# Optimization experiments

Hardware: AMD Instinct MI355X
Metric: run time of the kernel (lower is better)

The kernel has to match this reference:

```python
import jax, jax.numpy as jnp
import numpy as np

L, E, K = 2, 8, 2  # num_layers, num_experts, top_k
B, S, I, H = 4, 512, 768, 768


def gru_seq(x_seq, h0, Wih, Whh, bih, bhh):
    """PyTorch-semantics GRU over [B,S,H]. Returns (outputs [B,S,H], h_last [B,H])."""
    def step(h, x_t):
        gi = x_t @ Wih.T + bih          # [B,3H]
        gh = h @ Whh.T + bhh            # [B,3H]
        i_r, i_z, i_n = jnp.split(gi, 3, axis=-1)
        h_r, h_z, h_n = jnp.split(gh, 3, axis=-1)
        r = jax.nn.sigmoid(i_r + h_r)
        z = jax.nn.sigmoid(i_z + h_z)
        n = jnp.tanh(i_n + r * h_n)
        h_new = (1.0 - z) * n + z * h
        return h_new, h_new
    h_last, ys = jax.lax.scan(step, h0, jnp.swapaxes(x_seq, 0, 1))  # scan over S
    return jnp.swapaxes(ys, 0, 1), h_last


def setup_inputs() -> dict:
    key = jax.random.key(0)
    ks = jax.random.split(key, 16)
    sc_in = 1.0 / np.sqrt(I)
    sc_h = 1.0 / np.sqrt(H)
    sc_ff = 1.0 / np.sqrt(4 * I)
    return {
        "x": jax.random.normal(ks[0], (B, S, I), jnp.float32),
        "proj_W": jax.random.normal(ks[1], (L, H, I), jnp.float32) * sc_in,
        "proj_b": jnp.zeros((L, H), jnp.float32),
        "gru_Wih": jax.random.normal(ks[2], (3 * H, H), jnp.float32) * sc_h,
        "gru_Whh": jax.random.normal(ks[3], (3 * H, H), jnp.float32) * sc_h,
        "gru_bih": jnp.zeros((3 * H,), jnp.float32),
        "gru_bhh": jnp.zeros((3 * H,), jnp.float32),
        "router_W": jax.random.normal(ks[4], (L, E, H), jnp.float32) * sc_h,
        "router_b": jnp.zeros((L, E), jnp.float32),
        "exp_W1": jax.random.normal(ks[5], (L, E, 4 * I, I), jnp.float32) * sc_in,
        "exp_b1": jnp.zeros((L, E, 4 * I), jnp.float32),
        "exp_W2": jax.random.normal(ks[6], (L, E, I, 4 * I), jnp.float32) * sc_ff,
        "exp_b2": jnp.zeros((L, E, I), jnp.float32),
    }


def reference(x, proj_W, proj_b, gru_Wih, gru_Whh, gru_bih, gru_bhh,
              router_W, router_b, exp_W1, exp_b1, exp_W2, exp_b2):
    h_state = jnp.zeros((B, H), x.dtype)  # GRU state carried across layers
    for l in range(L):
        # layer projection -> recurrent router state
        h_in = x @ proj_W[l].T + proj_b[l]                       # [B,S,H]
        h_seq, h_state = gru_seq(h_in, h_state, gru_Wih, gru_Whh, gru_bih, gru_bhh)
        # top-k routing over experts
        logits = h_seq @ router_W[l].T + router_b[l]             # [B,S,E]
        vals, idx = jax.lax.top_k(logits, K)                     # [B,S,K]
        gates_k = jax.nn.softmax(vals, axis=-1)                  # renormalized over top-k
        gate = jnp.sum(gates_k[..., None] * jax.nn.one_hot(idx, E, dtype=x.dtype), axis=-2)  # [B,S,E]
        # dense-masked expert compute (small fixed E)
        out = jnp.zeros_like(x)
        for e in range(E):
            h1 = jax.nn.relu(x @ exp_W1[l, e].T + exp_b1[l, e])  # [B,S,4I]
            ye = h1 @ exp_W2[l, e].T + exp_b2[l, e]              # [B,S,I]
            out = out + gate[..., e:e + 1] * ye
        x = out
    return x
```

## Files before the change

### kernel.cpp

```cpp
#include <hip/hip_runtime.h>
#include <cmath>

#define AGENT __HIP_MEMORY_SCOPE_AGENT


typedef __attribute__((ext_vector_type(8))) short short8;
typedef __attribute__((ext_vector_type(4))) float f32x4;

__global__ void reset_kernel(int* __restrict__ flags, int* __restrict__ counts,
                             float* __restrict__ hbuf0) {
  int i = blockIdx.x * 256 + threadIdx.x;
  if (i < 6208) flags[i] = 0;
  if (i < 16) counts[i] = 0;
  if (i < 3072) hbuf0[i] = 0.f;
}

__global__ __launch_bounds__(256)
void split_kernel(const float* __restrict__ in, short* __restrict__ hi,
                  short* __restrict__ lo, int n4) {
  int i = blockIdx.x * 256 + threadIdx.x;
  if (i >= n4) return;
  float4 v = ((const float4*)in)[i];
  unsigned ua = __float_as_uint(v.x), ub = __float_as_uint(v.y);
  unsigned uc = __float_as_uint(v.z), ud = __float_as_uint(v.w);
  unsigned ha = ua & 0xFFFF0000u, hb = ub & 0xFFFF0000u;
  unsigned hc = uc & 0xFFFF0000u, hd = ud & 0xFFFF0000u;
  unsigned hp0 = (ua >> 16) | hb;
  unsigned hp1 = (uc >> 16) | hd;
  float la = v.x - __uint_as_float(ha), lb = v.y - __uint_as_float(hb);
  float lc = v.z - __uint_as_float(hc), ld = v.w - __uint_as_float(hd);
  unsigned lp0 = (__float_as_uint(la) >> 16) | (__float_as_uint(lb) & 0xFFFF0000u);
  unsigned lp1 = (__float_as_uint(lc) >> 16) | (__float_as_uint(ld) & 0xFFFF0000u);
  ((uint2*)hi)[i] = make_uint2(hp0, hp1);
  ((uint2*)lo)[i] = make_uint2(lp0, lp1);
}

template<bool GI2>
__global__ __launch_bounds__(256)
void gemm_nt(const float* __restrict__ A, const float* __restrict__ Bw,
             const float* __restrict__ bias, float* __restrict__ C,
             int Kd, int lda, int ldc)
{
  __shared__ float As[16][132];
  __shared__ float Bs[16][132];

  int mbase = blockIdx.y * 128;
  int nbase = blockIdx.x * 128;
  int tid = threadIdx.x;
  int tx = tid & 15, ty = tid >> 4;

  const float* ap[2];
  const float* bp[2];
  int ldst[2];
#pragma unroll
  for (int i = 0; i < 2; ++i) {
    int v = tid + 256 * i;
    int row = v >> 2, kq = v & 3;
    ap[i] = A + (size_t)(mbase + row) * lda + kq * 4;
    bp[i] = Bw + (size_t)(nbase + row) * Kd + kq * 4;
    ldst[i] = kq * 4 * 132 + row;
  }

  float acc[8][8];
#pragma unroll
  for (int i = 0; i < 8; ++i)
#pragma unroll
    for (int j = 0; j < 8; ++j) acc[i][j] = 0.f;

  for (int kb = 0; kb < Kd; kb += 16) {
    float4 av[2], bv[2];
#pragma unroll
    for (int i = 0; i < 2; ++i) {
      av[i] = *(const float4*)(ap[i] + kb);
      bv[i] = *(const float4*)(bp[i] + kb);
    }
    if (kb) __syncthreads();
#pragma unroll
    for (int i = 0; i < 2; ++i) {
      float* ad = &As[0][0] + ldst[i];
      ad[0] = av[i].x; ad[132] = av[i].y; ad[264] = av[i].z; ad[396] = av[i].w;
      float* bd = &Bs[0][0] + ldst[i];
      bd[0] = bv[i].x; bd[132] = bv[i].y; bd[264] = bv[i].z; bd[396] = bv[i].w;
    }
    __syncthreads();
#pragma unroll
    for (int kk = 0; kk < 16; ++kk) {
      float a[8], b[8];
      *(float4*)&a[0] = *(const float4*)&As[kk][ty * 4];
      *(float4*)&a[4] = *(const float4*)&As[kk][ty * 4 + 64];
      *(float4*)&b[0] = *(const float4*)&Bs[kk][tx * 4];
      *(float4*)&b[4] = *(const float4*)&Bs[kk][tx * 4 + 64];
#pragma unroll
      for (int i = 0; i < 8; ++i)
#pragma unroll
        for (int j = 0; j < 8; ++j)
          acc[i][j] = fmaf(a[i], b[j], acc[i][j]);
    }
  }

#pragma unroll
  for (int i = 0; i < 8; ++i) {
    int lrow = ty * 4 + (i & 3) + ((i >> 2) << 6);
    int grow = mbase + lrow;
#pragma unroll
    for (int q = 0; q < 2; ++q) {
      int col = nbase + tx * 4 + (q << 6);
      float4 bb = *(const float4*)&bias[col];
      float4 st = make_float4(acc[i][q * 4 + 0] + bb.x, acc[i][q * 4 + 1] + bb.y,
                              acc[i][q * 4 + 2] + bb.z, acc[i][q * 4 + 3] + bb.w);
      if constexpr (GI2) {
        int t = grow & 511, bb2 = grow >> 9;
        int gate = col / 768, jj = col - gate * 768;
        int wg2 = jj >> 3, o = jj & 7;
        float* dst = C + ((((size_t)t * 96 + wg2) * 4 + bb2) * 3 + gate) * 8 + o;
        *(float4*)dst = st;
      } else {
        *(float4*)&C[(size_t)grow * ldc + col] = st;
      }
    }
  }
}

template<bool SHIFT, bool RELU, bool GATE, bool OUTSPLIT>
__global__ __launch_bounds__(256)
void gemm_mfma(const short* __restrict__ Ah_g, const short* __restrict__ Al_g,
               const float* __restrict__ Bw, const float* __restrict__ bias,
               float* __restrict__ C, short* __restrict__ Ch,
               short* __restrict__ Cl, int Kd, int lda, int ldc,
               const int* __restrict__ list, const int* __restrict__ count,
               const float* __restrict__ gates, long wstride, int bstride)
{
  __shared__ __align__(16) short Ah[128][40];
  __shared__ __align__(16) short Al[128][40];
  __shared__ __align__(16) short Bh[128][40];
  __shared__ __align__(16) short Bl[128][40];
  __shared__ int rowlist[128];

  int e = blockIdx.z;
  int cnt = count[e];
  int mbase = blockIdx.y * 128;
  if (mbase >= cnt) return;
  int nbase = blockIdx.x * 128;
  const float* Bp = Bw + (size_t)e * (size_t)wstride;
  const float* biasp = bias + (size_t)e * (size_t)bstride;

  int tid = threadIdx.x;
  if (tid < 128) {
    int r = mbase + tid;
    rowlist[tid] = list[e * 4096 + (r < cnt ? r : cnt - 1)];
  }
  __syncthreads();

  int arow = tid >> 1, ahalf = tid & 1;
  int aidx0 = rowlist[arow];
  int sr = SHIFT ? (aidx0 >> 1) : aidx0;
  const short* aph = Ah_g + (size_t)sr * lda + ahalf * 16;
  const short* apl = Al_g + (size_t)sr * lda + ahalf * 16;
  const float* bp = Bp + (size_t)(nbase + arow) * Kd + ahalf * 16;

  int wave = tid >> 6, lane = tid & 63;
  int wr = (wave >> 1) * 64, wc = (wave & 1) * 64;
  int fr = lane & 15, fo = (lane >> 4) * 8;

  f32x4 acc[4][4];
#pragma unroll
  for (int i = 0; i < 4; ++i)
#pragma unroll
    for (int j = 0; j < 4; ++j) acc[i][j] = f32x4{0.f, 0.f, 0.f, 0.f};

  for (int kb = 0; kb < Kd; kb += 32) {
    uint4 a_h0 = *(const uint4*)(aph + kb);
    uint4 a_h1 = *(const uint4*)(aph + kb + 8);
    uint4 a_l0 = *(const uint4*)(apl + kb);
    uint4 a_l1 = *(const uint4*)(apl + kb + 8);
    float4 b0 = *(const float4*)(bp + kb);
    float4 b1 = *(const float4*)(bp + kb + 4);
    float4 b2 = *(const float4*)(bp + kb + 8);
    float4 b3 = *(const float4*)(bp + kb + 12);
    if (kb) __syncthreads();
    *(uint4*)&Ah[arow][ahalf * 16] = a_h0;
    *(uint4*)&Ah[arow][ahalf * 16 + 8] = a_h1;
    *(uint4*)&Al[arow][ahalf * 16] = a_l0;
    *(uint4*)&Al[arow][ahalf * 16 + 8] = a_l1;
    unsigned hp[8], lp[8];
    const float4 bbv[4] = {b0, b1, b2, b3};
#pragma unroll
    for (int q = 0; q < 4; ++q) {
      unsigned ua = __float_as_uint(bbv[q].x), ub = __float_as_uint(bbv[q].y);
      unsigned uc = __float_as_uint(bbv[q].z), ud = __float_as_uint(bbv[q].w);
      unsigned ha = ua & 0xFFFF0000u, hb = ub & 0xFFFF0000u;
      unsigned hc = uc & 0xFFFF0000u, hd = ud & 0xFFFF0000u;
      hp[q * 2] = (ua >> 16) | hb;
      hp[q * 2 + 1] = (uc >> 16) | hd;
      float la = bbv[q].x - __uint_as_float(ha);
      float lb = bbv[q].y - __uint_as_float(hb);
      float lc = bbv[q].z - __uint_as_float(hc);
      float ld = bbv[q].w - __uint_as_float(hd);
      lp[q * 2] = (__float_as_uint(la) >> 16) | (__float_as_uint(lb) & 0xFFFF0000u);
      lp[q * 2 + 1] = (__float_as_uint(lc) >> 16) | (__float_as_uint(ld) & 0xFFFF0000u);
    }
    *(uint4*)&Bh[arow][ahalf * 16] = make_uint4(hp[0], hp[1], hp[2], hp[3]);
    *(uint4*)&Bh[arow][ahalf * 16 + 8] = make_uint4(hp[4], hp[5], hp[6], hp[7]);
    *(uint4*)&Bl[arow][ahalf * 16] = make_uint4(lp[0], lp[1], lp[2], lp[3]);
    *(uint4*)&Bl[arow][ahalf * 16 + 8] = make_uint4(lp[4], lp[5], lp[6], lp[7]);
    __syncthreads();

    short8 fah[4], fal[4], fbh[4], fbl[4];
#pragma unroll
    for (int mt = 0; mt < 4; ++mt) {
      fah[mt] = *(const short8*)&Ah[wr + mt * 16 + fr][fo];
      fal[mt] = *(const short8*)&Al[wr + mt * 16 + fr][fo];
    }
#pragma unroll
    for (int nt = 0; nt < 4; ++nt) {
      fbh[nt] = *(const short8*)&Bh[wc + nt * 16 + fr][fo];
      fbl[nt] = *(const short8*)&Bl[wc + nt * 16 + fr][fo];
    }
#pragma unroll
    for (int mt = 0; mt < 4; ++mt)
#pragma unroll
      for (int nt = 0; nt < 4; ++nt) {
        acc[mt][nt] = __builtin_amdgcn_mfma_f32_16x16x32_bf16(fah[mt], fbh[nt], acc[mt][nt], 0, 0, 0);
        acc[mt][nt] = __builtin_amdgcn_mfma_f32_16x16x32_bf16(fah[mt], fbl[nt], acc[mt][nt], 0, 0, 0);
        acc[mt][nt] = __builtin_amdgcn_mfma_f32_16x16x32_bf16(fal[mt], fbh[nt], acc[mt][nt], 0, 0, 0);
      }
  }

  int crow = (lane >> 4) * 4;
#pragma unroll
  for (int mt = 0; mt < 4; ++mt) {
#pragma unroll
    for (int q = 0; q < 4; ++q) {
      int lrow = wr + mt * 16 + crow + q;
      int grow = mbase + lrow;
      if (grow < cnt) {
        int aidx = rowlist[lrow];
#pragma unroll
        for (int nt = 0; nt < 4; ++nt) {
          int col = nbase + wc + nt * 16 + fr;
          float v = acc[mt][nt][q] + biasp[col];
          if (RELU) v = fmaxf(v, 0.f);
          if (GATE) v *= gates[aidx];
          if (OUTSPLIT) {
            unsigned u = __float_as_uint(v);
            unsigned h = u & 0xFFFF0000u;
            Ch[(size_t)aidx * ldc + col] = (short)(u >> 16);
            float l2 = v - __uint_as_float(h);
            Cl[(size_t)aidx * ldc + col] = (short)(__float_as_uint(l2) >> 16);
          } else {
            C[(size_t)aidx * ldc + col] = v;
          }
        }
      }
    }
  }
}

__global__ __launch_bounds__(512)
void gru_kernel(const float* __restrict__ gi2, float* __restrict__ h_seq,
                float* __restrict__ hbuf, const float* __restrict__ Whh,
                const float* __restrict__ bhh,
                int* __restrict__ tags, int stepBase)
{
  const int H = 768, S = 512;
  __shared__ float hs[3072];
  int wg = blockIdx.x;
  int tid = threadIdx.x;
  int wave = tid >> 6;
  int lane = tid & 63;
  int j = wg * 8 + wave;

  float W[3][12];
#pragma unroll
  for (int g = 0; g < 3; ++g) {
    const float* wp = Whh + (size_t)(g * H + j) * H + lane * 4;
    *(float4*)&W[g][0] = *(const float4*)(wp);
    *(float4*)&W[g][4] = *(const float4*)(wp + 256);
    *(float4*)&W[g][8] = *(const float4*)(wp + 512);
  }
  float bh_r = bhh[j], bh_z = bhh[H + j], bh_n = bhh[2 * H + j];

  float h_own = 0.f;
  if (lane < 4)
    h_own = __hip_atomic_load(&hbuf[(stepBase & 1) * 3072 + lane * H + j],
                              __ATOMIC_RELAXED, AGENT);

  for (int tl = 0; tl < S; ++tl) {
    int g = stepBase + tl;
    const float* hb = hbuf + (g & 1) * 3072;
    float* hw = hbuf + ((g + 1) & 1) * 3072;

    float gv = 0.f;
    if (lane < 12)
      gv = gi2[(((size_t)tl * 96 + wg) * 12 + ((lane & 3) * 3 + (lane >> 2))) * 8 + wave];

    if (wave == 0) {
      for (;;) {
        int v1 = __hip_atomic_load(&tags[lane * 32], __ATOMIC_RELAXED, AGENT);
        int v2 = (lane < 32)
            ? __hip_atomic_load(&tags[(64 + lane) * 32], __ATOMIC_RELAXED, AGENT)
            : 0x7fffffff;
        if (__all(v1 >= g && v2 >= g)) break;
        __builtin_amdgcn_s_sleep(4);
      }
    }
    __syncthreads();

    float4 a, b4v;
    asm volatile("global_load_dwordx4 %0, %1, off sc0 sc1"
                 : "=v"(a) : "v"(hb + tid * 4) : "memory");
    if (tid < 256)
      asm volatile("global_load_dwordx4 %0, %1, off sc0 sc1"
                   : "=v"(b4v) : "v"(hb + 2048 + tid * 4) : "memory");
    asm volatile("s_waitcnt vmcnt(0)" ::: "memory");
    __builtin_amdgcn_sched_barrier(0);
    *(float4*)&hs[tid * 4] = a;
    if (tid < 256) *(float4*)&hs[2048 + tid * 4] = b4v;
    __syncthreads();

    if (tl >= 1) {
      if (wg < 64) {
        int rel = tid - wg * 8;
        if (rel >= 0 && rel < 8) {
          int i0 = tid * 4, bb = i0 / 768, d = i0 - bb * 768;
          *(float4*)&h_seq[((size_t)bb * S + (tl - 1)) * H + d] = a;
        }
      } else {
        int rel = tid - (wg - 64) * 8;
        if (rel >= 0 && rel < 8) {
          int i1 = 2048 + tid * 4, bb1 = i1 / 768, d1 = i1 - bb1 * 768;
          *(float4*)&h_seq[((size_t)bb1 * S + (tl - 1)) * H + d1] = b4v;
        }
      }
    }

    float hseg[4][12];
#pragma unroll
    for (int b4 = 0; b4 < 4; ++b4) {
      *(float4*)&hseg[b4][0] = *(const float4*)&hs[b4 * 768 + lane * 4];
      *(float4*)&hseg[b4][4] = *(const float4*)&hs[b4 * 768 + 256 + lane * 4];
      *(float4*)&hseg[b4][8] = *(const float4*)&hs[b4 * 768 + 512 + lane * 4];
    }

    float acc[3][4];
#pragma unroll
    for (int gg = 0; gg < 3; ++gg)
#pragma unroll
      for (int b4 = 0; b4 < 4; ++b4) {
        float s = 0.f;
#pragma unroll
        for (int i = 0; i < 12; ++i) s = fmaf(W[gg][i], hseg[b4][i], s);
        acc[gg][b4] = s;
      }
#pragma unroll
    for (int gg = 0; gg < 3; ++gg)
#pragma unroll
      for (int b4 = 0; b4 < 4; ++b4) {
        float v = acc[gg][b4];
#pragma unroll
        for (int m = 32; m >= 1; m >>= 1) v += __shfl_xor(v, m);
        acc[gg][b4] = v;
      }

    float gi_r = __shfl(gv, (lane & 3));
    float gi_z = __shfl(gv, 4 + (lane & 3));
    float gi_n = __shfl(gv, 8 + (lane & 3));

    if (lane < 4) {
      float ar = acc[0][0], az = acc[1][0], an = acc[2][0];
      if (lane == 1) { ar = acc[0][1]; az = acc[1][1]; an = acc[2][1]; }
      if (lane == 2) { ar = acc[0][2]; az = acc[1][2]; an = acc[2][2]; }
      if (lane == 3) { ar = acc[0][3]; az = acc[1][3]; an = acc[2][3]; }
      float r = 1.f / (1.f + expf(-(gi_r + ar + bh_r)));
      float z = 1.f / (1.f + expf(-(gi_z + az + bh_z)));
      float n = tanhf(gi_n + r * (an + bh_n));
      float hn = (1.f - z) * n + z * h_own;
      h_own = hn;
      __hip_atomic_store(&hw[lane * H + j], hn, __ATOMIC_RELAXED, AGENT);
    }

    asm volatile("s_waitcnt vmcnt(0)" ::: "memory");
    __syncthreads();
    if (tid == 0)
      __hip_atomic_store(&tags[wg * 32], g + 1, __ATOMIC_RELAXED, AGENT);
  }

  if (lane < 4)
    h_seq[((size_t)lane * S + (S - 1)) * H + j] = h_own;
}

__global__ __launch_bounds__(64)
void router_kernel(const float* __restrict__ h_seq, const float* __restrict__ rW,
                   const float* __restrict__ rb, int* __restrict__ counts,
                   int* __restrict__ lists, float* __restrict__ gates)
{
  int t = blockIdx.x;
  int lane = threadIdx.x;
  const float* hp = h_seq + (size_t)t * 768 + lane * 12;
  float h[12];
  *(float4*)&h[0] = *(const float4*)(hp);
  *(float4*)&h[4] = *(const float4*)(hp + 4);
  *(float4*)&h[8] = *(const float4*)(hp + 8);

  float lg[8];
#pragma unroll
  for (int e = 0; e < 8; ++e) {
    const float* wp = rW + e * 768 + lane * 12;
    float s = 0.f;
#pragma unroll
    for (int i = 0; i < 12; ++i) s = fmaf(h[i], wp[i], s);
#pragma unroll
    for (int m = 32; m >= 1; m >>= 1) s += __shfl_xor(s, m);
    lg[e] = s + rb[e];
  }
  if (lane == 0) {
    float v1 = lg[0]; int e1 = 0;
#pragma unroll
    for (int e = 1; e < 8; ++e) {
      if (lg[e] > v1) { v1 = lg[e]; e1 = e; }
    }
    float v2 = -INFINITY; int es = 0;
#pragma unroll
    for (int e = 0; e < 8; ++e) {
      if (e != e1 && lg[e] > v2) { v2 = lg[e]; es = e; }
    }
    float ed = expf(v2 - v1);
    float g1 = 1.f / (1.f + ed);
    float g2 = ed / (1.f + ed);
    int a0 = t * 2, a1 = t * 2 + 1;
    gates[a0] = g1;
    gates[a1] = g2;
    int p = atomicAdd(&counts[e1], 1);
    lists[e1 * 4096 + p] = a0;
    p = atomicAdd(&counts[es], 1);
    lists[es * 4096 + p] = a1;
  }
}

__global__ __launch_bounds__(256)
void combine_kernel(const float* __restrict__ ybuf, float* __restrict__ out)
{
  int i = blockIdx.x * 256 + threadIdx.x;
  int fi = i * 4;
  int t = fi / 768;
  int d = fi % 768;
  float4 y0 = *(const float4*)&ybuf[(size_t)(2 * t) * 768 + d];
  float4 y1 = *(const float4*)&ybuf[(size_t)(2 * t + 1) * 768 + d];
  float4 r = make_float4(y0.x + y1.x, y0.y + y1.y, y0.z + y1.z, y0.w + y1.w);
  *(float4*)&out[fi] = r;
}

extern "C" void kernel_launch(void* const* d_in, const int* in_sizes, int n_in,
                              void* d_out, int out_size, void* d_ws, size_t ws_size,
                              hipStream_t stream) {
  (void)in_sizes; (void)n_in; (void)out_size; (void)ws_size;
  const float* x      = (const float*)d_in[0];
  const float* proj_W = (const float*)d_in[1];
  const float* proj_b = (const float*)d_in[2];
  const float* Wih    = (const float*)d_in[3];
  const float* Whh    = (const float*)d_in[4];
  const float* bih    = (const float*)d_in[5];
  const float* bhh    = (const float*)d_in[6];
  const float* rW     = (const float*)d_in[7];
  const float* rb     = (const float*)d_in[8];
  const float* eW1    = (const float*)d_in[9];
  const float* eb1    = (const float*)d_in[10];
  const float* eW2    = (const float*)d_in[11];
  const float* eb2    = (const float*)d_in[12];
  float* out = (float*)d_out;

  float* f = (float*)d_ws;
  float* h_in  = f;
  float* gi2   = h_in + 1572864;
  float* h_seq = gi2 + 4718592;
  float* x_buf = h_seq + 1572864;
  float* ybuf  = x_buf + 1572864;
  float* hbuf  = ybuf + 3145728;
  float* gates = hbuf + 6144;
  short* xh    = (short*)(gates + 4096);
  short* xl    = xh + 1572864;
  short* H1h   = xl + 1572864;
  short* H1l   = H1h + 12582912;
  int* ints    = (int*)(H1l + 12582912);
  int* counts  = ints;
  int* lists   = ints + 16;
  int* tags    = ints + 16 + 32768;

  reset_kernel<<<25, 256, 0, stream>>>(tags, counts, hbuf);

  for (int l = 0; l < 2; ++l) {
    const float* xin = l ? x_buf : x;

    dim3 g1(6, 16);
    gemm_nt<false><<<g1, 256, 0, stream>>>(
        xin, proj_W + (size_t)l * 768 * 768, proj_b + l * 768, h_in,
        768, 768, 768);

    dim3 g2(18, 16);
    gemm_nt<true><<<g2, 256, 0, stream>>>(
        h_in, Wih, bih, gi2, 768, 768, 0);

    gru_kernel<<<96, 512, 0, stream>>>(gi2, h_seq, hbuf, Whh, bhh,
                                       tags, l * 512);

    router_kernel<<<2048, 64, 0, stream>>>(h_seq, rW + (size_t)l * 8 * 768,
                                           rb + l * 8, counts + l * 8, lists, gates);

    split_kernel<<<1536, 256, 0, stream>>>(xin, xh, xl, 393216);

    dim3 ga(24, 32, 8);
    gemm_mfma<true, true, false, true><<<ga, 256, 0, stream>>>(
        xh, xl, eW1 + (size_t)l * 8 * 3072 * 768, eb1 + (size_t)l * 8 * 3072,
        nullptr, H1h, H1l, 768, 768, 3072,
        lists, counts + l * 8, nullptr, (long)3072 * 768, 3072);

    dim3 gb(6, 32, 8);
    gemm_mfma<false, false, true, false><<<gb, 256, 0, stream>>>(
        H1h, H1l, eW2 + (size_t)l * 8 * 768 * 3072, eb2 + (size_t)l * 8 * 768,
        ybuf, nullptr, nullptr, 3072, 3072, 768,
        lists, counts + l * 8, gates, (long)768 * 3072, 768);

    combine_kernel<<<1536, 256, 0, stream>>>(ybuf, l ? out : x_buf);
  }
}
```

Baseline: 6.070 ms.

## Partition GRU workgroups by batch to shrink cross-block synchronization groups

The GRU recurrence kernel now assigns each batch row to its own group of 24 workgroups, each wave computing 4 hidden columns for one batch instead of one column for all 4 batches. Each workgroup then polls only 24 peer flags instead of 96 and loads only its batch's 768-element hidden state per step, which cuts the per-step barrier and load cost on the latency-bound serial loop. The gi projection layout is rearranged to match, and the sleep interval in the spin loop is shortened. In exchange each wave holds four times as many Whh weights in registers, which raises register pressure, and each weight row is now read by four batch groups.

```diff
diff --git a/kernel.cpp b/kernel.cpp
--- a/kernel.cpp
+++ b/kernel.cpp
@@ -35,7 +35,7 @@
   ((uint2*)lo)[i] = make_uint2(lp0, lp1);
 }
 
-template<bool GI2>
+template<bool GI3>
 __global__ __launch_bounds__(256)
 void gemm_nt(const float* __restrict__ A, const float* __restrict__ Bw,
              const float* __restrict__ bias, float* __restrict__ C,
@@ -108,11 +108,11 @@
       float4 bb = *(const float4*)&bias[col];
       float4 st = make_float4(acc[i][q * 4 + 0] + bb.x, acc[i][q * 4 + 1] + bb.y,
                               acc[i][q * 4 + 2] + bb.z, acc[i][q * 4 + 3] + bb.w);
-      if constexpr (GI2) {
+      if constexpr (GI3) {
         int t = grow & 511, bb2 = grow >> 9;
         int gate = col / 768, jj = col - gate * 768;
-        int wg2 = jj >> 3, o = jj & 7;
-        float* dst = C + ((((size_t)t * 96 + wg2) * 4 + bb2) * 3 + gate) * 8 + o;
+        int wv = jj >> 2;
+        float* dst = C + ((((size_t)t * 4 + bb2) * 192 + wv) * 12 + gate * 4);
         *(float4*)dst = st;
       } else {
         *(float4*)&C[(size_t)grow * ldc + col] = st;
@@ -256,110 +256,95 @@
   }
 }
 
-__global__ __launch_bounds__(512)
-void gru_kernel(const float* __restrict__ gi2, float* __restrict__ h_seq,
+__global__ __launch_bounds__(512, 2)
+void gru_kernel(const float* __restrict__ gi3, float* __restrict__ h_seq,
                 float* __restrict__ hbuf, const float* __restrict__ Whh,
                 const float* __restrict__ bhh,
                 int* __restrict__ tags, int stepBase)
 {
   const int H = 768, S = 512;
-  __shared__ float hs[3072];
+  __shared__ float hs[768];
   int wg = blockIdx.x;
+  int b = wg / 24;
+  int wgi = wg - b * 24;
   int tid = threadIdx.x;
   int wave = tid >> 6;
   int lane = tid & 63;
-  int j = wg * 8 + wave;
-
-  float W[3][12];
-#pragma unroll
-  for (int g = 0; g < 3; ++g) {
-    const float* wp = Whh + (size_t)(g * H + j) * H + lane * 4;
-    *(float4*)&W[g][0] = *(const float4*)(wp);
-    *(float4*)&W[g][4] = *(const float4*)(wp + 256);
-    *(float4*)&W[g][8] = *(const float4*)(wp + 512);
-  }
-  float bh_r = bhh[j], bh_z = bhh[H + j], bh_n = bhh[2 * H + j];
+  int wv = wgi * 8 + wave;
+
+  float W[4][3][12];
+#pragma unroll
+  for (int c = 0; c < 4; ++c)
+#pragma unroll
+    for (int g = 0; g < 3; ++g) {
+      const float* wp = Whh + (size_t)(g * H + wv * 4 + c) * H + lane * 4;
+      *(float4*)&W[c][g][0] = *(const float4*)(wp);
+      *(float4*)&W[c][g][4] = *(const float4*)(wp + 256);
+      *(float4*)&W[c][g][8] = *(const float4*)(wp + 512);
+    }
+  int mycol = wv * 4 + (lane & 3);
+  float bh_r = bhh[mycol], bh_z = bhh[H + mycol], bh_n = bhh[2 * H + mycol];
 
   float h_own = 0.f;
   if (lane < 4)
-    h_own = __hip_atomic_load(&hbuf[(stepBase & 1) * 3072 + lane * H + j],
+    h_own = __hip_atomic_load(&hbuf[(stepBase & 1) * 3072 + b * H + mycol],
                               __ATOMIC_RELAXED, AGENT);
 
   for (int tl = 0; tl < S; ++tl) {
     int g = stepBase + tl;
-    const float* hb = hbuf + (g & 1) * 3072;
-    float* hw = hbuf + ((g + 1) & 1) * 3072;
+    const float* hb = hbuf + (g & 1) * 3072 + b * H;
+    float* hw = hbuf + ((g + 1) & 1) * 3072 + b * H;
 
     float gv = 0.f;
     if (lane < 12)
-      gv = gi2[(((size_t)tl * 96 + wg) * 12 + ((lane & 3) * 3 + (lane >> 2))) * 8 + wave];
+      gv = gi3[((((size_t)tl * 4 + b) * 192 + wv) * 12) + lane];
 
     if (wave == 0) {
       for (;;) {
-        int v1 = __hip_atomic_load(&tags[lane * 32], __ATOMIC_RELAXED, AGENT);
-        int v2 = (lane < 32)
-            ? __hip_atomic_load(&tags[(64 + lane) * 32], __ATOMIC_RELAXED, AGENT)
+        int v1 = (lane < 24)
+            ? __hip_atomic_load(&tags[(b * 24 + lane) * 32], __ATOMIC_RELAXED, AGENT)
             : 0x7fffffff;
-        if (__all(v1 >= g && v2 >= g)) break;
-        __builtin_amdgcn_s_sleep(4);
+        if (__all(v1 >= g)) break;
+        __builtin_amdgcn_s_sleep(2);
       }
     }
     __syncthreads();
 
-    float4 a, b4v;
-    asm volatile("global_load_dwordx4 %0, %1, off sc0 sc1"
-                 : "=v"(a) : "v"(hb + tid * 4) : "memory");
-    if (tid < 256)
+    float4 a = make_float4(0.f, 0.f, 0.f, 0.f);
+    if (tid < 192)
       asm volatile("global_load_dwordx4 %0, %1, off sc0 sc1"
-                   : "=v"(b4v) : "v"(hb + 2048 + tid * 4) : "memory");
+                   : "=v"(a) : "v"(hb + tid * 4) : "memory");
     asm volatile("s_waitcnt vmcnt(0)" ::: "memory");
     __builtin_amdgcn_sched_barrier(0);
-    *(float4*)&hs[tid * 4] = a;
-    if (tid < 256) *(float4*)&hs[2048 + tid * 4] = b4v;
+    if (tid < 192) *(float4*)&hs[tid * 4] = a;
     __syncthreads();
 
-    if (tl >= 1) {
-      if (wg < 64) {
-        int rel = tid - wg * 8;
-        if (rel >= 0 && rel < 8) {
-          int i0 = tid * 4, bb = i0 / 768, d = i0 - bb * 768;
-          *(float4*)&h_seq[((size_t)bb * S + (tl - 1)) * H + d] = a;
-        }
-      } else {
-        int rel = tid - (wg - 64) * 8;
-        if (rel >= 0 && rel < 8) {
-          int i1 = 2048 + tid * 4, bb1 = i1 / 768, d1 = i1 - bb1 * 768;
-          *(float4*)&h_seq[((size_t)bb1 * S + (tl - 1)) * H + d1] = b4v;
-        }
+    if (tl >= 1 && tid >= wgi * 8 && tid < wgi * 8 + 8)
+      *(float4*)&h_seq[((size_t)b * S + (tl - 1)) * H + tid * 4] = a;
+
+    float hseg[12];
+    *(float4*)&hseg[0] = *(const float4*)&hs[lane * 4];
+    *(float4*)&hseg[4] = *(const float4*)&hs[256 + lane * 4];
+    *(float4*)&hseg[8] = *(const float4*)&hs[512 + lane * 4];
+
+    float acc[4][3];
+#pragma unroll
+    for (int c = 0; c < 4; ++c)
+#pragma unroll
+      for (int gg = 0; gg < 3; ++gg) {
+        float s = 0.f;
+#pragma unroll
+        for (int i = 0; i < 12; ++i) s = fmaf(W[c][gg][i], hseg[i], s);
+        acc[c][gg] = s;
       }
-    }
-
-    float hseg[4][12];
-#pragma unroll
-    for (int b4 = 0; b4 < 4; ++b4) {
-      *(float4*)&hseg[b4][0] = *(const float4*)&hs[b4 * 768 + lane * 4];
-      *(float4*)&hseg[b4][4] = *(const float4*)&hs[b4 * 768 + 256 + lane * 4];
-      *(float4*)&hseg[b4][8] = *(const float4*)&hs[b4 * 768 + 512 + lane * 4];
-    }
-
-    float acc[3][4];
-#pragma unroll
-    for (int gg = 0; gg < 3; ++gg)
-#pragma unroll
-      for (int b4 = 0; b4 < 4; ++b4) {
-        float s = 0.f;
-#pragma unroll
-        for (int i = 0; i < 12; ++i) s = fmaf(W[gg][i], hseg[b4][i], s);
-        acc[gg][b4] = s;
-      }
-#pragma unroll
-    for (int gg = 0; gg < 3; ++gg)
-#pragma unroll
-      for (int b4 = 0; b4 < 4; ++b4) {
-        float v = acc[gg][b4];
+#pragma unroll
+    for (int c = 0; c < 4; ++c)
+#pragma unroll
+      for (int gg = 0; gg < 3; ++gg) {
+        float v = acc[c][gg];
 #pragma unroll
         for (int m = 32; m >= 1; m >>= 1) v += __shfl_xor(v, m);
-        acc[gg][b4] = v;
+        acc[c][gg] = v;
       }
 
     float gi_r = __shfl(gv, (lane & 3));
@@ -367,26 +352,26 @@
     float gi_n = __shfl(gv, 8 + (lane & 3));
 
     if (lane < 4) {
-      float ar = acc[0][0], az = acc[1][0], an = acc[2][0];
-      if (lane == 1) { ar = acc[0][1]; az = acc[1][1]; an = acc[2][1]; }
-      if (lane == 2) { ar = acc[0][2]; az = acc[1][2]; an = acc[2][2]; }
-      if (lane == 3) { ar = acc[0][3]; az = acc[1][3]; an = acc[2][3]; }
+      float ar = acc[0][0], az = acc[0][1], an = acc[0][2];
+      if (lane == 1) { ar = acc[1][0]; az = acc[1][1]; an = acc[1][2]; }
+      if (lane == 2) { ar = acc[2][0]; az = acc[2][1]; an = acc[2][2]; }
+      if (lane == 3) { ar = acc[3][0]; az = acc[3][1]; an = acc[3][2]; }
       float r = 1.f / (1.f + expf(-(gi_r + ar + bh_r)));
       float z = 1.f / (1.f + expf(-(gi_z + az + bh_z)));
       float n = tanhf(gi_n + r * (an + bh_n));
       float hn = (1.f - z) * n + z * h_own;
       h_own = hn;
-      __hip_atomic_store(&hw[lane * H + j], hn, __ATOMIC_RELAXED, AGENT);
+      __hip_atomic_store(&hw[mycol], hn, __ATOMIC_RELAXED, AGENT);
     }
 
     asm volatile("s_waitcnt vmcnt(0)" ::: "memory");
     __syncthreads();
     if (tid == 0)
-      __hip_atomic_store(&tags[wg * 32], g + 1, __ATOMIC_RELAXED, AGENT);
+      __hip_atomic_store(&tags[(b * 24 + wgi) * 32], g + 1, __ATOMIC_RELAXED, AGENT);
   }
 
   if (lane < 4)
-    h_seq[((size_t)lane * S + (S - 1)) * H + j] = h_own;
+    h_seq[((size_t)b * S + (S - 1)) * H + mycol] = h_own;
 }
 
 __global__ __launch_bounds__(64)
@@ -471,8 +456,8 @@
 
   float* f = (float*)d_ws;
   float* h_in  = f;
-  float* gi2   = h_in + 1572864;
-  float* h_seq = gi2 + 4718592;
+  float* gi3   = h_in + 1572864;
+  float* h_seq = gi3 + 4718592;
   float* x_buf = h_seq + 1572864;
   float* ybuf  = x_buf + 1572864;
   float* hbuf  = ybuf + 3145728;
@@ -498,9 +483,9 @@
 
     dim3 g2(18, 16);
     gemm_nt<true><<<g2, 256, 0, stream>>>(
-        h_in, Wih, bih, gi2, 768, 768, 0);
-
-    gru_kernel<<<96, 512, 0, stream>>>(gi2, h_seq, hbuf, Whh, bhh,
+        h_in, Wih, bih, gi3, 768, 768, 0);
+
+    gru_kernel<<<96, 512, 0, stream>>>(gi3, h_seq, hbuf, Whh, bhh,
                                        tags, l * 512);
 
     router_kernel<<<2048, 64, 0, stream>>>(h_seq, rW + (size_t)l * 8 * 768,
```

New measurement: 5.449 ms. 10.2% less time.
